# Kernel tuning notes

Hardware: AMD Instinct MI355X
Metric: run time of the kernel (lower is better)

Reference implementation:

```python
import jax, jax.numpy as jnp
import numpy as np

B, T, D, H = 1, 2049, 1024, 16
HD = D // H                      # head_dim = 64
MAX_SEQ = 1025
L = 2 * MAX_SEQ - 1              # = T (required by the module's relative shift)

def setup_inputs() -> dict:
    key = jax.random.key(0)
    ks = jax.random.split(key, 12)
    s = 0.02
    return {
        'q': jax.random.normal(ks[0], (B, T, D), dtype=jnp.float32),
        'k': jax.random.normal(ks[1], (B, T, D), dtype=jnp.float32),
        'v': jax.random.normal(ks[2], (B, T, D), dtype=jnp.float32),
        'mask': jnp.tril(jnp.ones((1, 1, T, T), dtype=jnp.int32)),  # causal
        'Wq_w': jax.random.normal(ks[3], (D, D), dtype=jnp.float32) * s,
        'Wq_b': jnp.zeros((D,), dtype=jnp.float32),
        'Wk_w': jax.random.normal(ks[4], (D, D), dtype=jnp.float32) * s,
        'Wk_b': jnp.zeros((D,), dtype=jnp.float32),
        'Wv_w': jax.random.normal(ks[5], (D, D), dtype=jnp.float32) * s,
        'Wv_b': jnp.zeros((D,), dtype=jnp.float32),
        'Er': jax.random.normal(ks[6], (L, HD), dtype=jnp.float32),
        'Wo_w': jax.random.normal(ks[7], (D, D), dtype=jnp.float32) * s,
        'Wo_b': jnp.zeros((D,), dtype=jnp.float32),
    }

def reference(q, k, v, mask, Wq_w, Wq_b, Wk_w, Wk_b, Wv_w, Wv_b, Er, Wo_w, Wo_b):
    b, t, d = q.shape
    def proj(x, w, bias):
        # nn.Linear: x @ W^T + b ; then (B,T,H,HD) -> (B,H,T,HD)
        return (x @ w.T + bias).reshape(b, t, H, HD).transpose(0, 2, 1, 3)
    qh = proj(q, Wq_w, Wq_b)
    kh = proj(k, Wk_w, Wk_b)
    vh = proj(v, Wv_w, Wv_b)
    scores = jnp.einsum('bhtd,bhsd->bhts', qh, kh)          # (B,H,T,T)
    QEr = jnp.einsum('bhtd,ld->bhtl', qh, Er)               # (B,H,T,L) with L == T
    # _relative_shift: pad a zero row on seq dim then drop first row ->
    # row i becomes QEr row i+1, last row zeros (faithful to torch code)
    rel = jnp.concatenate([QEr[:, :, 1:, :], jnp.zeros_like(QEr[:, :, :1, :])], axis=2)
    scores = scores + rel
    scores = jnp.where(mask[:, :, :t, :t] == 0, -jnp.inf, scores)
    attn = jax.nn.softmax(scores / (HD ** 0.5), axis=-1)
    ctx = jnp.einsum('bhts,bhsd->bthd', attn, vh).reshape(b, t, d)
    return ctx @ Wo_w.T + Wo_b
```

## Files before the change

kernel.cpp:

```cpp
#include <hip/hip_runtime.h>
#include <hip/hip_bf16.h>
#include <math.h>

constexpr int T_SEQ = 2049;
constexpr int D_MODEL = 1024;
constexpr int N_HEAD = 16;
constexpr int HEAD_DIM = 64;
constexpr int VT_STRIDE = 2112;
constexpr int T1_ROWS = 1152;

typedef __attribute__((ext_vector_type(8))) short short8;
typedef __attribute__((ext_vector_type(4))) short short4v;
typedef __attribute__((ext_vector_type(4))) float floatx4;

__device__ inline void load_lds16(const void* g, void* l) {
  __builtin_amdgcn_global_load_lds(
      (const __attribute__((address_space(1))) unsigned int*)g,
      (__attribute__((address_space(3))) unsigned int*)l, 16, 0, 0);
}

__device__ inline short8 cvt8_bf16(const float* p) {
  float4 a = *(const float4*)p, b = *(const float4*)(p + 4);
  __hip_bfloat16 t[8] = {__float2bfloat16(a.x), __float2bfloat16(a.y),
                         __float2bfloat16(a.z), __float2bfloat16(a.w),
                         __float2bfloat16(b.x), __float2bfloat16(b.y),
                         __float2bfloat16(b.z), __float2bfloat16(b.w)};
  return *(const short8*)t;
}

__device__ inline float bf2f(__hip_bfloat16 x) { return __bfloat162float(x); }

__global__ __launch_bounds__(256) void cast_all(
    const float* __restrict__ q, const float* __restrict__ k,
    const float* __restrict__ v, const float* __restrict__ wq,
    const float* __restrict__ wk, const float* __restrict__ wv,
    const float* __restrict__ wo, __hip_bfloat16* __restrict__ qo,
    __hip_bfloat16* __restrict__ ko, __hip_bfloat16* __restrict__ vo,
    __hip_bfloat16* __restrict__ wqo, __hip_bfloat16* __restrict__ wko,
    __hip_bfloat16* __restrict__ wvo, __hip_bfloat16* __restrict__ woo) {
  const int z = blockIdx.y;
  const float* in;
  __hip_bfloat16* out;
  int n;
  switch (z) {
    case 0: in = q; out = qo; n = T_SEQ * D_MODEL; break;
    case 1: in = k; out = ko; n = T_SEQ * D_MODEL; break;
    case 2: in = v; out = vo; n = T_SEQ * D_MODEL; break;
    case 3: in = wq; out = wqo; n = D_MODEL * D_MODEL; break;
    case 4: in = wk; out = wko; n = D_MODEL * D_MODEL; break;
    case 5: in = wv; out = wvo; n = D_MODEL * D_MODEL; break;
    default: in = wo; out = woo; n = D_MODEL * D_MODEL; break;
  }
  const int i = (blockIdx.x * 256 + threadIdx.x) * 8;
  if (i + 8 > n) return;
  *(short8*)(out + i) = cvt8_bf16(in + i);
}

template <int BN, int OUTK>
__global__ __launch_bounds__(256) void mfma_gemm(
    const __hip_bfloat16* __restrict__ A0, const __hip_bfloat16* __restrict__ A1,
    const __hip_bfloat16* __restrict__ A2, const __hip_bfloat16* __restrict__ W0,
    const __hip_bfloat16* __restrict__ W1, const __hip_bfloat16* __restrict__ W2,
    const float* __restrict__ bias0, const float* __restrict__ bias1,
    const float* __restrict__ bias2, void* C0, void* C1, void* C2, int M) {
  constexpr int K = D_MODEL;
  constexpr int NT = BN / 32;
  __shared__ __align__(16) __hip_bfloat16 As[2][64 * 64];
  __shared__ __align__(16) __hip_bfloat16 Bs[2][BN * 64];

  const int z = blockIdx.z;
  const short* A = (const short*)(z == 0 ? A0 : z == 1 ? A1 : A2);
  const short* W = (const short*)(z == 0 ? W0 : z == 1 ? W1 : W2);
  const float* bias = z == 0 ? bias0 : z == 1 ? bias1 : bias2;
  void* C = z == 0 ? C0 : z == 1 ? C1 : C2;

  const int tid = threadIdx.x;
  const int wave = tid >> 6, lane = tid & 63;
  const int col = lane & 15, quad = lane >> 4;
  const int wm = wave >> 1, wn = wave & 1;
  const int m0 = blockIdx.y * 64, n0 = blockIdx.x * BN;

  const int srow = lane >> 3;
  const int sslot = lane & 7;
  const int sch = sslot ^ srow;

  floatx4 acc[2][NT];
#pragma unroll
  for (int i = 0; i < 2; i++)
#pragma unroll
    for (int j = 0; j < NT; j++) acc[i][j] = (floatx4){0.f, 0.f, 0.f, 0.f};

#define GSTAGE(K0, BUF)                                                     \
  {                                                                         \
    _Pragma("unroll") for (int ii = 0; ii < 2; ii++) {                      \
      const int rb = (wave * 2 + ii) * 8;                                   \
      const int am = min(m0 + rb + srow, M - 1);                            \
      load_lds16(A + (size_t)am * K + (K0) + sch * 8,                       \
                 (char*)&As[BUF][0] + rb * 128);                            \
    }                                                                       \
    _Pragma("unroll") for (int ii = 0; ii < BN / 32; ii++) {                \
      const int rb = (wave * (BN / 32) + ii) * 8;                           \
      const int bn = n0 + rb + srow;                                        \
      load_lds16(W + (size_t)bn * K + (K0) + sch * 8,                       \
                 (char*)&Bs[BUF][0] + rb * 128);                            \
    }                                                                       \
  }

  GSTAGE(0, 0)
  int buf = 0;

  for (int kb = 0; kb < K / 64; ++kb, buf ^= 1) {
    __syncthreads();
    if (kb + 1 < K / 64) GSTAGE((kb + 1) * 64, buf ^ 1)

    const __hip_bfloat16* as = &As[buf][0];
    const __hip_bfloat16* bs = &Bs[buf][0];
#pragma unroll
    for (int kk = 0; kk < 2; kk++) {
      short8 af[2], bf[NT];
#pragma unroll
      for (int t = 0; t < 2; t++) {
        const int ra = wm * 32 + t * 16 + col;
        af[t] = *(const short8*)(as + ra * 64 + ((kk * 4 + quad) ^ (ra & 7)) * 8);
      }
#pragma unroll
      for (int t = 0; t < NT; t++) {
        const int rb = wn * (BN / 2) + t * 16 + col;
        bf[t] = *(const short8*)(bs + rb * 64 + ((kk * 4 + quad) ^ (rb & 7)) * 8);
      }
#pragma unroll
      for (int mt = 0; mt < 2; mt++)
#pragma unroll
        for (int nt = 0; nt < NT; nt++)
          acc[mt][nt] = __builtin_amdgcn_mfma_f32_16x16x32_bf16(af[mt], bf[nt],
                                                                acc[mt][nt], 0, 0, 0);
    }
  }

#pragma unroll
  for (int mt = 0; mt < 2; mt++) {
#pragma unroll
    for (int r = 0; r < 4; r++) {
      const int m = m0 + wm * 32 + mt * 16 + quad * 4 + r;
      if (m >= M) continue;
#pragma unroll
      for (int nt = 0; nt < NT; nt++) {
        const int n = n0 + wn * (BN / 2) + nt * 16 + col;
        const float val = acc[mt][nt][r] + bias[n];
        if (OUTK == 0) {
          ((float*)C)[(size_t)m * D_MODEL + n] = val;
        } else {
          if (z < 2) {
            const int h = n >> 6, hd = n & 63;
            ((__hip_bfloat16*)C)[((size_t)h * T_SEQ + m) * HEAD_DIM + hd] =
                __float2bfloat16(val);
          } else {
            ((__hip_bfloat16*)C)[(size_t)m * D_MODEL + n] = __float2bfloat16(val);
          }
        }
      }
    }
  }
}

__global__ __launch_bounds__(256) void transpose_v_er(
    const __hip_bfloat16* __restrict__ vpr, __hip_bfloat16* __restrict__ vt,
    const float* __restrict__ Er, __hip_bfloat16* __restrict__ er_bf) {
  const int tid = threadIdx.x;
  if (blockIdx.y == 16) {
    const int i = (blockIdx.x * 256 + tid) * 8;
    if (i + 8 <= T_SEQ * HEAD_DIM) *(short8*)(er_bf + i) = cvt8_bf16(Er + i);
    return;
  }
  if (blockIdx.x >= 33) return;

  __shared__ __align__(16) __hip_bfloat16 tile[64][72];
  const int t0 = blockIdx.x * 64;
  const int h = blockIdx.y;
  const short* plane = (const short*)vpr;
  short* oplane = (short*)(vt + (size_t)h * HEAD_DIM * VT_STRIDE);

  for (int idx = tid; idx < 64 * 8; idx += 256) {
    const int row = idx >> 3, ch = idx & 7;
    const int t = t0 + row;
    short8 v = {0, 0, 0, 0, 0, 0, 0, 0};
    if (t < T_SEQ) v = *(const short8*)(plane + (size_t)t * D_MODEL + h * 64 + ch * 8);
    *(short8*)&tile[row][ch * 8] = v;
  }
  __syncthreads();
  for (int idx = tid; idx < 64 * 8; idx += 256) {
    const int d = idx >> 3, ch = idx & 7;
    short8 v;
#pragma unroll
    for (int i = 0; i < 8; i++) v[i] = *(const short*)&tile[ch * 8 + i][d];
    *(short8*)(oplane + (size_t)d * VT_STRIDE + t0 + ch * 8) = v;
  }
}

__global__ __launch_bounds__(512, 4) void flash_attn(
    const __hip_bfloat16* __restrict__ qh, const __hip_bfloat16* __restrict__ kh,
    const __hip_bfloat16* __restrict__ er, const __hip_bfloat16* __restrict__ vt,
    __hip_bfloat16* __restrict__ ctx, __hip_bfloat16* __restrict__ O0,
    __hip_bfloat16* __restrict__ O1, float* __restrict__ l0g,
    float* __restrict__ l1g) {
  __shared__ __align__(16) __hip_bfloat16 Ks[2][64 * 128];
  __shared__ __align__(16) __hip_bfloat16 Vs[2][64 * 64];
  __shared__ __align__(16) __hip_bfloat16 Ps[8][1024];

  const int tid = threadIdx.x;
  const int h = blockIdx.y;
  const int b = blockIdx.x;

  const int qt = (b < 8) ? b : 8 + ((b - 8) >> 1);
  const int tq0 = qt * 128;
  const int jmax = min(tq0 + 127, T_SEQ - 1) >> 6;
  int j0, j1;
  bool alt;
  if (b < 8) {
    j0 = 0; j1 = jmax; alt = false;
  } else {
    const int mid = (jmax + 1) >> 1;
    alt = (b - 8) & 1;
    j0 = alt ? mid : 0;
    j1 = alt ? jmax : mid - 1;
  }

  const int wave = tid >> 6;
  const int lane = tid & 63;
  const int col = lane & 15;
  const int quad = lane >> 4;

  const short* qplane = (const short*)(qh + (size_t)h * T_SEQ * HEAD_DIM);
  const short* kplane = (const short*)(kh + (size_t)h * T_SEQ * HEAD_DIM);
  const short* eplane = (const short*)er;
  const short* vplane = (const short*)(vt + (size_t)h * HEAD_DIM * VT_STRIDE);

  const int t_abs = tq0 + wave * 16 + col;
  const int tload = min(t_abs, T_SEQ - 1);
  const bool hiz = (t_abs >= T_SEQ - 1);
  short8 aq[4];
#pragma unroll
  for (int kc = 0; kc < 4; kc++) {
    short8 v = *(const short8*)(qplane + (size_t)tload * 64 + kc * 32 + quad * 8);
    if (kc >= 2 && hiz) v = (short8){0, 0, 0, 0, 0, 0, 0, 0};
    aq[kc] = v;
  }

  floatx4 o[4];
  float l_lane = 0.f;
#pragma unroll
  for (int i = 0; i < 4; i++) o[i] = (floatx4){0.f, 0.f, 0.f, 0.f};

  const int tstrip = tq0 + wave * 16;
  __hip_bfloat16* psw = &Ps[wave][0];

#define STAGE_TILE(JJ, BUF)                                                        \
  {                                                                                \
    const int s0_ = (JJ) * 64;                                                     \
    _Pragma("unroll") for (int ii = 0; ii < 2; ii++) {                             \
      const int i_ = wave * 2 + ii;                                                \
      const int r_ = i_ * 4 + (lane >> 4);                                         \
      const int sl_ = lane & 15;                                                   \
      const int g_ = (sl_ & 8) | ((sl_ ^ (r_ & 7)) & 7);                           \
      const int s_ = min(s0_ + r_, T_SEQ - 1);                                     \
      const short* src_ = (g_ < 8) ? (kplane + (size_t)s_ * 64 + g_ * 8)           \
                                   : (eplane + (size_t)s_ * 64 + (g_ - 8) * 8);    \
      load_lds16(src_, (char*)&Ks[BUF][0] + i_ * 1024);                            \
    }                                                                              \
    {                                                                              \
      const int d_ = wave * 8 + (lane >> 3);                                       \
      const int sl_ = lane & 7;                                                    \
      const int g_ = sl_ ^ (d_ & 7);                                               \
      load_lds16(vplane + (size_t)d_ * VT_STRIDE + s0_ + g_ * 8,                   \
                 (char*)&Vs[BUF][0] + wave * 1024);                                \
    }                                                                              \
  }

  STAGE_TILE(j0, 0)
  int buf = 0;

  for (int j = j0; j <= j1; ++j, buf ^= 1) {
    __syncthreads();
    if (j < j1) STAGE_TILE(j + 1, buf ^ 1)

    const int s0 = j * 64;
    if (s0 > tstrip + 15) continue;

    const __hip_bfloat16* ks = &Ks[buf][0];
    const __hip_bfloat16* vs = &Vs[buf][0];

    floatx4 sacc[4];
#pragma unroll
    for (int st = 0; st < 4; st++) {
      floatx4 c = {0.f, 0.f, 0.f, 0.f};
      const int row = st * 16 + col;
#pragma unroll
      for (int kc = 0; kc < 4; kc++) {
        const int ch = kc * 4 + quad;
        const int slot = (ch & 8) | ((ch ^ (row & 7)) & 7);
        short8 ka = *(const short8*)(ks + row * 128 + slot * 8);
        c = __builtin_amdgcn_mfma_f32_16x16x32_bf16(ka, aq[kc], c, 0, 0, 0);
      }
      sacc[st] = c;
    }

    if (s0 + 63 > tstrip) {
#pragma unroll
      for (int st = 0; st < 4; st++) {
        const int sbase = s0 + st * 16 + quad * 4;
#pragma unroll
        for (int r = 0; r < 4; r++)
          if (sbase + r > t_abs) sacc[st][r] = -INFINITY;
      }
    }

    float rs = 0.f;
#pragma unroll
    for (int st = 0; st < 4; st++)
#pragma unroll
      for (int r = 0; r < 4; r++) {
        const float p = __expf(sacc[st][r] * 0.125f);
        sacc[st][r] = p;
        rs += p;
      }
    l_lane += rs;

#pragma unroll
    for (int st = 0; st < 4; st++) {
      __hip_bfloat16 pb[4];
#pragma unroll
      for (int r = 0; r < 4; r++) pb[r] = __float2bfloat16(sacc[st][r]);
      const int kcA = st >> 1;
      const int quadA = (st & 1) * 2 + (quad >> 1);
      const int off = ((kcA * 4 + quadA) * 16 + col) * 8 + (quad & 1) * 4;
      *(short4v*)(psw + off) = *(const short4v*)pb;
    }
    short8 pa[2];
#pragma unroll
    for (int kc = 0; kc < 2; kc++)
      pa[kc] = *(const short8*)(psw + ((kc * 4 + quad) * 16 + col) * 8);

#pragma unroll
    for (int nt = 0; nt < 4; nt++) {
      const int row = nt * 16 + col;
#pragma unroll
      for (int kc = 0; kc < 2; kc++) {
        const int slot = (kc * 4 + quad) ^ (row & 7);
        short8 vb = *(const short8*)(vs + row * 64 + slot * 8);
        o[nt] = __builtin_amdgcn_mfma_f32_16x16x32_bf16(pa[kc], vb, o[nt], 0, 0, 0);
      }
    }
  }

  l_lane += __shfl_xor(l_lane, 16, 64);
  l_lane += __shfl_xor(l_lane, 32, 64);

  if (b < 8) {
    const float linv = 1.0f / l_lane;
    float linv_r[4];
#pragma unroll
    for (int r = 0; r < 4; r++) linv_r[r] = __shfl(linv, quad * 4 + r, 64);
#pragma unroll
    for (int r = 0; r < 4; r++) {
      const int t = tstrip + quad * 4 + r;
#pragma unroll
      for (int nt = 0; nt < 4; nt++)
        ctx[(size_t)t * D_MODEL + h * 64 + nt * 16 + col] =
            __float2bfloat16(o[nt][r] * linv_r[r]);
    }
  } else {
    if (lane < 16) {
      const int t = tstrip + lane;
      if (t < T_SEQ) {
        if (!alt)
          l0g[h * T1_ROWS + (t - 1024)] = l_lane;
        else
          l1g[h * T1_ROWS + (t - 1024)] = l_lane;
      }
    }
#pragma unroll
    for (int r = 0; r < 4; r++) {
      const int t = tstrip + quad * 4 + r;
      if (t < T_SEQ) {
        __hip_bfloat16* dst = (!alt ? O0 : O1) + (size_t)(t - 1024) * D_MODEL;
#pragma unroll
        for (int nt = 0; nt < 4; nt++)
          dst[h * 64 + nt * 16 + col] = __float2bfloat16(o[nt][r]);
      }
    }
  }
}

__global__ __launch_bounds__(256) void finalize(
    const __hip_bfloat16* __restrict__ O0, const __hip_bfloat16* __restrict__ O1,
    const float* __restrict__ l0g, const float* __restrict__ l1g,
    __hip_bfloat16* __restrict__ ctx) {
  const int idx = blockIdx.x * 256 + threadIdx.x;
  const int tr = idx >> 7;
  const int t = 1024 + tr;
  if (t >= T_SEQ) return;
  const int ch = idx & 127;
  const int h = ch >> 3;

  const float l = l0g[h * T1_ROWS + tr] + l1g[h * T1_ROWS + tr];
  const __hip_bfloat16* a = O0 + (size_t)tr * D_MODEL + ch * 8;
  const __hip_bfloat16* bsrc = O1 + (size_t)tr * D_MODEL + ch * 8;
  const float inv = 1.0f / l;
  __hip_bfloat16 outv[8];
#pragma unroll
  for (int i = 0; i < 8; i++)
    outv[i] = __float2bfloat16((bf2f(a[i]) + bf2f(bsrc[i])) * inv);
  *(short8*)(ctx + (size_t)t * D_MODEL + ch * 8) = *(const short8*)outv;
}

extern "C" void kernel_launch(void* const* d_in, const int* in_sizes, int n_in,
                              void* d_out, int out_size, void* d_ws, size_t ws_size,
                              hipStream_t stream) {
  const float* q = (const float*)d_in[0];
  const float* k = (const float*)d_in[1];
  const float* v = (const float*)d_in[2];
  const float* Wq_w = (const float*)d_in[4];
  const float* Wq_b = (const float*)d_in[5];
  const float* Wk_w = (const float*)d_in[6];
  const float* Wk_b = (const float*)d_in[7];
  const float* Wv_w = (const float*)d_in[8];
  const float* Wv_b = (const float*)d_in[9];
  const float* Er = (const float*)d_in[10];
  const float* Wo_w = (const float*)d_in[11];
  const float* Wo_b = (const float*)d_in[12];
  float* out = (float*)d_out;

  char* ws = (char*)d_ws;
  const size_t sz_plane = (size_t)T_SEQ * D_MODEL * 2;
  const size_t sz_w = (size_t)D_MODEL * D_MODEL * 2;
  __hip_bfloat16* qbf = (__hip_bfloat16*)ws;
  __hip_bfloat16* kbf = (__hip_bfloat16*)(ws + sz_plane);
  __hip_bfloat16* vbf = (__hip_bfloat16*)(ws + 2 * sz_plane);
  char* wbase = ws + 3 * sz_plane;
  __hip_bfloat16* wob = (__hip_bfloat16*)(wbase);
  __hip_bfloat16* wqb = (__hip_bfloat16*)(wbase + sz_w);
  __hip_bfloat16* wkb = (__hip_bfloat16*)(wbase + 2 * sz_w);
  __hip_bfloat16* wvb = (__hip_bfloat16*)(wbase + 3 * sz_w);
  char* pbase = wbase + 4 * sz_w;
  __hip_bfloat16* qpr = (__hip_bfloat16*)(pbase);
  __hip_bfloat16* kpr = (__hip_bfloat16*)(pbase + sz_plane);
  __hip_bfloat16* vpr = (__hip_bfloat16*)(pbase + 2 * sz_plane);

  const size_t sz_vt = (size_t)N_HEAD * HEAD_DIM * VT_STRIDE * 2;
  const size_t sz_er = (size_t)T_SEQ * HEAD_DIM * 2;
  const size_t sz_Op = (size_t)T1_ROWS * D_MODEL * 2;
  const size_t sz_l = (size_t)N_HEAD * T1_ROWS * 4;
  __hip_bfloat16* vt = (__hip_bfloat16*)ws;
  __hip_bfloat16* er_bf = (__hip_bfloat16*)(ws + sz_vt);
  __hip_bfloat16* O0 = (__hip_bfloat16*)(ws + sz_vt + sz_er);
  __hip_bfloat16* O1 = (__hip_bfloat16*)(ws + sz_vt + sz_er + sz_Op);
  float* l0g = (float*)(ws + sz_vt + sz_er + 2 * sz_Op);
  float* l1g = (float*)(ws + sz_vt + sz_er + 2 * sz_Op + sz_l);
  __hip_bfloat16* ctxb = (__hip_bfloat16*)(wbase + sz_w);

  const dim3 blk(256);

  cast_all<<<dim3(1025, 7), blk, 0, stream>>>(q, k, v, Wq_w, Wk_w, Wv_w, Wo_w, qbf,
                                              kbf, vbf, wqb, wkb, wvb, wob);

  mfma_gemm<128, 2><<<dim3(8, 33, 3), blk, 0, stream>>>(
      qbf, kbf, vbf, wqb, wkb, wvb, Wq_b, Wk_b, Wv_b, qpr, kpr, vpr, T_SEQ);

  transpose_v_er<<<dim3(65, 17), blk, 0, stream>>>(vpr, vt, Er, er_bf);

  flash_attn<<<dim3(26, N_HEAD), dim3(512), 0, stream>>>(qpr, kpr, er_bf, vt, ctxb,
                                                         O0, O1, l0g, l1g);

  finalize<<<dim3((1025 * 128 + 255) / 256), blk, 0, stream>>>(O0, O1, l0g, l1g, ctxb);

  mfma_gemm<64, 0><<<dim3(16, 33, 1), blk, 0, stream>>>(
      ctxb, ctxb, ctxb, wob, wob, wob, Wo_b, Wo_b, Wo_b, out, out, out, T_SEQ);
}
```

Baseline: 208.6 us.

## Fuse V transpose into QKV GEMM epilogue, fold Er cast into cast kernel

The QKV projection GEMM now writes the V projection directly in transposed (head_dim x time) layout, so the separate transpose kernel and its intermediate buffer are removed. The Er fp32-to-bf16 conversion moves into the shared cast kernel as an eighth slice. The GEMM gains a BM template parameter, and the output projection switches to 128x64 tiles with half as many row blocks. The transposed V stores are narrow 4-element column writes, which may coalesce poorly, and the workspace layout is rewritten with 256-byte aligned carving.

```diff
diff --git a/kernel.cpp b/kernel.cpp
--- a/kernel.cpp
+++ b/kernel.cpp
@@ -34,10 +34,11 @@
     const float* __restrict__ q, const float* __restrict__ k,
     const float* __restrict__ v, const float* __restrict__ wq,
     const float* __restrict__ wk, const float* __restrict__ wv,
-    const float* __restrict__ wo, __hip_bfloat16* __restrict__ qo,
-    __hip_bfloat16* __restrict__ ko, __hip_bfloat16* __restrict__ vo,
-    __hip_bfloat16* __restrict__ wqo, __hip_bfloat16* __restrict__ wko,
-    __hip_bfloat16* __restrict__ wvo, __hip_bfloat16* __restrict__ woo) {
+    const float* __restrict__ wo, const float* __restrict__ er,
+    __hip_bfloat16* __restrict__ qo, __hip_bfloat16* __restrict__ ko,
+    __hip_bfloat16* __restrict__ vo, __hip_bfloat16* __restrict__ wqo,
+    __hip_bfloat16* __restrict__ wko, __hip_bfloat16* __restrict__ wvo,
+    __hip_bfloat16* __restrict__ woo, __hip_bfloat16* __restrict__ ero) {
   const int z = blockIdx.y;
   const float* in;
   __hip_bfloat16* out;
@@ -49,14 +50,15 @@
     case 3: in = wq; out = wqo; n = D_MODEL * D_MODEL; break;
     case 4: in = wk; out = wko; n = D_MODEL * D_MODEL; break;
     case 5: in = wv; out = wvo; n = D_MODEL * D_MODEL; break;
-    default: in = wo; out = woo; n = D_MODEL * D_MODEL; break;
+    case 6: in = wo; out = woo; n = D_MODEL * D_MODEL; break;
+    default: in = er; out = ero; n = T_SEQ * HEAD_DIM; break;
   }
   const int i = (blockIdx.x * 256 + threadIdx.x) * 8;
   if (i + 8 > n) return;
   *(short8*)(out + i) = cvt8_bf16(in + i);
 }
 
-template <int BN, int OUTK>
+template <int BM, int BN, int OUTK>
 __global__ __launch_bounds__(256) void mfma_gemm(
     const __hip_bfloat16* __restrict__ A0, const __hip_bfloat16* __restrict__ A1,
     const __hip_bfloat16* __restrict__ A2, const __hip_bfloat16* __restrict__ W0,
@@ -64,8 +66,9 @@
     const float* __restrict__ bias0, const float* __restrict__ bias1,
     const float* __restrict__ bias2, void* C0, void* C1, void* C2, int M) {
   constexpr int K = D_MODEL;
+  constexpr int MT = BM / 32;
   constexpr int NT = BN / 32;
-  __shared__ __align__(16) __hip_bfloat16 As[2][64 * 64];
+  __shared__ __align__(16) __hip_bfloat16 As[2][BM * 64];
   __shared__ __align__(16) __hip_bfloat16 Bs[2][BN * 64];
 
   const int z = blockIdx.z;
@@ -78,22 +81,22 @@
   const int wave = tid >> 6, lane = tid & 63;
   const int col = lane & 15, quad = lane >> 4;
   const int wm = wave >> 1, wn = wave & 1;
-  const int m0 = blockIdx.y * 64, n0 = blockIdx.x * BN;
+  const int m0 = blockIdx.y * BM, n0 = blockIdx.x * BN;
 
   const int srow = lane >> 3;
   const int sslot = lane & 7;
   const int sch = sslot ^ srow;
 
-  floatx4 acc[2][NT];
-#pragma unroll
-  for (int i = 0; i < 2; i++)
+  floatx4 acc[MT][NT];
+#pragma unroll
+  for (int i = 0; i < MT; i++)
 #pragma unroll
     for (int j = 0; j < NT; j++) acc[i][j] = (floatx4){0.f, 0.f, 0.f, 0.f};
 
 #define GSTAGE(K0, BUF)                                                     \
   {                                                                         \
-    _Pragma("unroll") for (int ii = 0; ii < 2; ii++) {                      \
-      const int rb = (wave * 2 + ii) * 8;                                   \
+    _Pragma("unroll") for (int ii = 0; ii < BM / 32; ii++) {                \
+      const int rb = (wave * (BM / 32) + ii) * 8;                           \
       const int am = min(m0 + rb + srow, M - 1);                            \
       load_lds16(A + (size_t)am * K + (K0) + sch * 8,                       \
                  (char*)&As[BUF][0] + rb * 128);                            \
@@ -117,10 +120,10 @@
     const __hip_bfloat16* bs = &Bs[buf][0];
 #pragma unroll
     for (int kk = 0; kk < 2; kk++) {
-      short8 af[2], bf[NT];
-#pragma unroll
-      for (int t = 0; t < 2; t++) {
-        const int ra = wm * 32 + t * 16 + col;
+      short8 af[MT], bf[NT];
+#pragma unroll
+      for (int t = 0; t < MT; t++) {
+        const int ra = wm * (BM / 2) + t * 16 + col;
         af[t] = *(const short8*)(as + ra * 64 + ((kk * 4 + quad) ^ (ra & 7)) * 8);
       }
 #pragma unroll
@@ -129,7 +132,7 @@
         bf[t] = *(const short8*)(bs + rb * 64 + ((kk * 4 + quad) ^ (rb & 7)) * 8);
       }
 #pragma unroll
-      for (int mt = 0; mt < 2; mt++)
+      for (int mt = 0; mt < MT; mt++)
 #pragma unroll
         for (int nt = 0; nt < NT; nt++)
           acc[mt][nt] = __builtin_amdgcn_mfma_f32_16x16x32_bf16(af[mt], bf[nt],
@@ -138,62 +141,40 @@
   }
 
 #pragma unroll
-  for (int mt = 0; mt < 2; mt++) {
-#pragma unroll
-    for (int r = 0; r < 4; r++) {
-      const int m = m0 + wm * 32 + mt * 16 + quad * 4 + r;
-      if (m >= M) continue;
-#pragma unroll
-      for (int nt = 0; nt < NT; nt++) {
-        const int n = n0 + wn * (BN / 2) + nt * 16 + col;
-        const float val = acc[mt][nt][r] + bias[n];
-        if (OUTK == 0) {
-          ((float*)C)[(size_t)m * D_MODEL + n] = val;
+  for (int mt = 0; mt < MT; mt++) {
+    const int mb = m0 + wm * (BM / 2) + mt * 16 + quad * 4;
+#pragma unroll
+    for (int nt = 0; nt < NT; nt++) {
+      const int n = n0 + wn * (BN / 2) + nt * 16 + col;
+      if (OUTK == 2 && z == 2) {
+        __hip_bfloat16 pb[4];
+#pragma unroll
+        for (int r = 0; r < 4; r++)
+          pb[r] = __float2bfloat16(acc[mt][nt][r] + bias[n]);
+        __hip_bfloat16* vrow = (__hip_bfloat16*)C + (size_t)n * VT_STRIDE;
+        if (mb + 4 <= M) {
+          *(short4v*)(vrow + mb) = *(const short4v*)pb;
         } else {
-          if (z < 2) {
+#pragma unroll
+          for (int r = 0; r < 4; r++)
+            if (mb + r < M) vrow[mb + r] = pb[r];
+        }
+      } else {
+#pragma unroll
+        for (int r = 0; r < 4; r++) {
+          const int m = mb + r;
+          if (m >= M) continue;
+          const float val = acc[mt][nt][r] + bias[n];
+          if (OUTK == 0) {
+            ((float*)C)[(size_t)m * D_MODEL + n] = val;
+          } else {
             const int h = n >> 6, hd = n & 63;
             ((__hip_bfloat16*)C)[((size_t)h * T_SEQ + m) * HEAD_DIM + hd] =
                 __float2bfloat16(val);
-          } else {
-            ((__hip_bfloat16*)C)[(size_t)m * D_MODEL + n] = __float2bfloat16(val);
           }
         }
       }
     }
-  }
-}
-
-__global__ __launch_bounds__(256) void transpose_v_er(
-    const __hip_bfloat16* __restrict__ vpr, __hip_bfloat16* __restrict__ vt,
-    const float* __restrict__ Er, __hip_bfloat16* __restrict__ er_bf) {
-  const int tid = threadIdx.x;
-  if (blockIdx.y == 16) {
-    const int i = (blockIdx.x * 256 + tid) * 8;
-    if (i + 8 <= T_SEQ * HEAD_DIM) *(short8*)(er_bf + i) = cvt8_bf16(Er + i);
-    return;
-  }
-  if (blockIdx.x >= 33) return;
-
-  __shared__ __align__(16) __hip_bfloat16 tile[64][72];
-  const int t0 = blockIdx.x * 64;
-  const int h = blockIdx.y;
-  const short* plane = (const short*)vpr;
-  short* oplane = (short*)(vt + (size_t)h * HEAD_DIM * VT_STRIDE);
-
-  for (int idx = tid; idx < 64 * 8; idx += 256) {
-    const int row = idx >> 3, ch = idx & 7;
-    const int t = t0 + row;
-    short8 v = {0, 0, 0, 0, 0, 0, 0, 0};
-    if (t < T_SEQ) v = *(const short8*)(plane + (size_t)t * D_MODEL + h * 64 + ch * 8);
-    *(short8*)&tile[row][ch * 8] = v;
-  }
-  __syncthreads();
-  for (int idx = tid; idx < 64 * 8; idx += 256) {
-    const int d = idx >> 3, ch = idx & 7;
-    short8 v;
-#pragma unroll
-    for (int i = 0; i < 8; i++) v[i] = *(const short*)&tile[ch * 8 + i][d];
-    *(short8*)(oplane + (size_t)d * VT_STRIDE + t0 + ch * 8) = v;
   }
 }
 
@@ -430,49 +411,46 @@
   const float* Wo_b = (const float*)d_in[12];
   float* out = (float*)d_out;
 
-  char* ws = (char*)d_ws;
+  char* p = (char*)d_ws;
+  auto carve = [&](size_t bytes) {
+    char* r = p;
+    p += (bytes + 255) & ~(size_t)255;
+    return r;
+  };
   const size_t sz_plane = (size_t)T_SEQ * D_MODEL * 2;
   const size_t sz_w = (size_t)D_MODEL * D_MODEL * 2;
-  __hip_bfloat16* qbf = (__hip_bfloat16*)ws;
-  __hip_bfloat16* kbf = (__hip_bfloat16*)(ws + sz_plane);
-  __hip_bfloat16* vbf = (__hip_bfloat16*)(ws + 2 * sz_plane);
-  char* wbase = ws + 3 * sz_plane;
-  __hip_bfloat16* wob = (__hip_bfloat16*)(wbase);
-  __hip_bfloat16* wqb = (__hip_bfloat16*)(wbase + sz_w);
-  __hip_bfloat16* wkb = (__hip_bfloat16*)(wbase + 2 * sz_w);
-  __hip_bfloat16* wvb = (__hip_bfloat16*)(wbase + 3 * sz_w);
-  char* pbase = wbase + 4 * sz_w;
-  __hip_bfloat16* qpr = (__hip_bfloat16*)(pbase);
-  __hip_bfloat16* kpr = (__hip_bfloat16*)(pbase + sz_plane);
-  __hip_bfloat16* vpr = (__hip_bfloat16*)(pbase + 2 * sz_plane);
-
-  const size_t sz_vt = (size_t)N_HEAD * HEAD_DIM * VT_STRIDE * 2;
-  const size_t sz_er = (size_t)T_SEQ * HEAD_DIM * 2;
-  const size_t sz_Op = (size_t)T1_ROWS * D_MODEL * 2;
-  const size_t sz_l = (size_t)N_HEAD * T1_ROWS * 4;
-  __hip_bfloat16* vt = (__hip_bfloat16*)ws;
-  __hip_bfloat16* er_bf = (__hip_bfloat16*)(ws + sz_vt);
-  __hip_bfloat16* O0 = (__hip_bfloat16*)(ws + sz_vt + sz_er);
-  __hip_bfloat16* O1 = (__hip_bfloat16*)(ws + sz_vt + sz_er + sz_Op);
-  float* l0g = (float*)(ws + sz_vt + sz_er + 2 * sz_Op);
-  float* l1g = (float*)(ws + sz_vt + sz_er + 2 * sz_Op + sz_l);
-  __hip_bfloat16* ctxb = (__hip_bfloat16*)(wbase + sz_w);
+  __hip_bfloat16* qbf = (__hip_bfloat16*)carve(sz_plane);
+  __hip_bfloat16* kbf = (__hip_bfloat16*)carve(sz_plane);
+  __hip_bfloat16* vbf = (__hip_bfloat16*)carve(sz_plane);
+  __hip_bfloat16* wqb = (__hip_bfloat16*)carve(sz_w);
+  __hip_bfloat16* wkb = (__hip_bfloat16*)carve(sz_w);
+  __hip_bfloat16* wvb = (__hip_bfloat16*)carve(sz_w);
+  __hip_bfloat16* wob = (__hip_bfloat16*)carve(sz_w);
+  __hip_bfloat16* qpr = (__hip_bfloat16*)carve(sz_plane);
+  __hip_bfloat16* kpr = (__hip_bfloat16*)carve(sz_plane);
+  __hip_bfloat16* vt =
+      (__hip_bfloat16*)carve((size_t)N_HEAD * HEAD_DIM * VT_STRIDE * 2);
+  __hip_bfloat16* er_bf = (__hip_bfloat16*)carve((size_t)T_SEQ * HEAD_DIM * 2);
+  __hip_bfloat16* O0 = (__hip_bfloat16*)carve((size_t)T1_ROWS * D_MODEL * 2);
+  __hip_bfloat16* O1 = (__hip_bfloat16*)carve((size_t)T1_ROWS * D_MODEL * 2);
+  float* l0g = (float*)carve((size_t)N_HEAD * T1_ROWS * 4);
+  float* l1g = (float*)carve((size_t)N_HEAD * T1_ROWS * 4);
+  __hip_bfloat16* ctxb = (__hip_bfloat16*)carve(sz_plane);
 
   const dim3 blk(256);
 
-  cast_all<<<dim3(1025, 7), blk, 0, stream>>>(q, k, v, Wq_w, Wk_w, Wv_w, Wo_w, qbf,
-                                              kbf, vbf, wqb, wkb, wvb, wob);
-
-  mfma_gemm<128, 2><<<dim3(8, 33, 3), blk, 0, stream>>>(
-      qbf, kbf, vbf, wqb, wkb, wvb, Wq_b, Wk_b, Wv_b, qpr, kpr, vpr, T_SEQ);
-
-  transpose_v_er<<<dim3(65, 17), blk, 0, stream>>>(vpr, vt, Er, er_bf);
+  cast_all<<<dim3(1025, 8), blk, 0, stream>>>(q, k, v, Wq_w, Wk_w, Wv_w, Wo_w, Er,
+                                              qbf, kbf, vbf, wqb, wkb, wvb, wob,
+                                              er_bf);
+
+  mfma_gemm<64, 128, 2><<<dim3(8, 33, 3), blk, 0, stream>>>(
+      qbf, kbf, vbf, wqb, wkb, wvb, Wq_b, Wk_b, Wv_b, qpr, kpr, vt, T_SEQ);
 
   flash_attn<<<dim3(26, N_HEAD), dim3(512), 0, stream>>>(qpr, kpr, er_bf, vt, ctxb,
                                                          O0, O1, l0g, l1g);
 
   finalize<<<dim3((1025 * 128 + 255) / 256), blk, 0, stream>>>(O0, O1, l0g, l1g, ctxb);
 
-  mfma_gemm<64, 0><<<dim3(16, 33, 1), blk, 0, stream>>>(
+  mfma_gemm<128, 64, 0><<<dim3(16, 17, 1), blk, 0, stream>>>(
       ctxb, ctxb, ctxb, wob, wob, wob, Wo_b, Wo_b, Wo_b, out, out, out, T_SEQ);
 }
```

Measured after the change: 208.4 us. No clear change (-0.1%).
